# Performance work log

Hardware: AMD Instinct MI355X
Metric: run time of the kernel (lower is better)

## Reference

```python
import jax, jax.numpy as jnp
import numpy as np

ALPHA = 32.0
LN_EPS = 1e-5

def _cdist(a, b):
    # a: [C, M, K], b: [C, N, K] -> [C, M, N] euclidean distances
    d2 = (jnp.sum(a * a, -1)[:, :, None]
          + jnp.sum(b * b, -1)[:, None, :]
          - 2.0 * jnp.einsum('cmk,cnk->cmn', a, b))
    return jnp.sqrt(jnp.maximum(d2, 1e-12))

def setup_inputs() -> dict:
    key = jax.random.key(0)
    k1, k2 = jax.random.split(key)
    B, D, H, W, C = 8, 16, 28, 28, 256
    CN, SS = 128, 28 * 28
    x = jax.random.normal(k1, (B, D, H, W, C), dtype=jnp.float32)
    ln_weight = jnp.ones((C,), dtype=jnp.float32)
    ln_bias = jnp.zeros((C,), dtype=jnp.float32)
    cluster_center = jax.random.uniform(k2, (C, CN, SS), dtype=jnp.float32)
    return {"x": x, "ln_weight": ln_weight, "ln_bias": ln_bias,
            "cluster_center": cluster_center}

def reference(x, ln_weight, ln_bias, cluster_center):
    B, D, H, W, C = x.shape
    CN = cluster_center.shape[1]
    # LayerNorm over last dim (feature_dim)
    mu = jnp.mean(x, -1, keepdims=True)
    var = jnp.mean(jnp.square(x - mu), -1, keepdims=True)
    xn = (x - mu) * jax.lax.rsqrt(var + LN_EPS) * ln_weight + ln_bias
    # B D H W C -> C (B D) (H W)
    x_re = jnp.transpose(xn, (4, 0, 1, 2, 3)).reshape(C, B * D, H * W)
    soft_assign = _cdist(x_re, cluster_center)          # [C, B*D, CN]
    # C (B D) CN -> B D C CN
    x_distance = jnp.transpose(soft_assign.reshape(C, B, D, CN), (1, 2, 0, 3))
    # NegSoftAssign: exp(-alpha*(x - min)) normalized == softmax(-alpha*x)
    x_distance_assign = jax.nn.softmax(-ALPHA * x_distance, axis=-1)
    cluster_dist = _cdist(cluster_center, cluster_center)  # [C, CN, CN]
    return (x_distance, x_distance_assign, cluster_dist)
```

## Files before the change

kernel.cpp:

```cpp
#include <hip/hip_runtime.h>
#include <hip/hip_bf16.h>
#include <math.h>

#define C_DIM 256
#define BD    128
#define HW    784
#define CN    128
#define KPAD  832
#define KTILES 26

typedef short bf16x8 __attribute__((ext_vector_type(8)));
typedef float f32x4 __attribute__((ext_vector_type(4)));

__device__ inline ushort f2b(float f) {
  unsigned u = __float_as_uint(f);
  unsigned r = (u + 0x7FFFu + ((u >> 16) & 1u)) >> 16;
  return (ushort)r;
}

__global__ __launch_bounds__(256) void ln_transpose_kernel(
    const float* __restrict__ x, const float* __restrict__ lnw,
    const float* __restrict__ lnb, ushort* __restrict__ xre,
    float* __restrict__ anorm) {
  __shared__ ushort btile[256 * 64];
  __shared__ float nbuf[4][256];
  const int t = threadIdx.x, bd = blockIdx.y, bx = blockIdx.x;
  const int hw0 = bx * 64;
  const int w = t >> 6, lane = t & 63;
  const int q = lane >> 4, l = lane & 15;
  const bool last = (bx == 12);
  const int ngroups = last ? 1 : 4;
  const int rpw = ngroups * 4;
  if (last) {
    for (int r = 16; r < 64; r += 4)
      *(ushort4*)&btile[t * 64 + r] = make_ushort4(0, 0, 0, 0);
  }
  float4 wv[4], bv[4];
  for (int s = 0; s < 4; ++s) {
    wv[s] = *(const float4*)(lnw + s * 64 + l * 4);
    bv[s] = *(const float4*)(lnb + s * 64 + l * 4);
  }
  float nrm[4][4];
  for (int s = 0; s < 4; ++s)
    for (int j = 0; j < 4; ++j) nrm[s][j] = 0.f;
  const float* xb = x + ((size_t)bd * HW + hw0) * 256 + l * 4;
  const int xr = l & 12;
  for (int g = 0; g < ngroups; ++g) {
    int r = w * rpw + g * 4 + q;
    float4 v[4];
    for (int s = 0; s < 4; ++s)
      v[s] = *(const float4*)(xb + (size_t)r * 256 + s * 64);
    float sum = 0.f, sq = 0.f;
    for (int s = 0; s < 4; ++s) {
      sum += v[s].x + v[s].y + v[s].z + v[s].w;
      sq = fmaf(v[s].x, v[s].x, sq); sq = fmaf(v[s].y, v[s].y, sq);
      sq = fmaf(v[s].z, v[s].z, sq); sq = fmaf(v[s].w, v[s].w, sq);
    }
    for (int off = 1; off <= 8; off <<= 1) {
      sum += __shfl_xor(sum, off, 64);
      sq  += __shfl_xor(sq, off, 64);
    }
    float mu = sum * (1.f / 256.f);
    float var = fmaf(-mu, mu, sq * (1.f / 256.f));
    float sc = rsqrtf(var + 1e-5f);
    int rp = r ^ xr;
    for (int s = 0; s < 4; ++s) {
      float y0 = (v[s].x - mu) * sc * wv[s].x + bv[s].x;
      float y1 = (v[s].y - mu) * sc * wv[s].y + bv[s].y;
      float y2 = (v[s].z - mu) * sc * wv[s].z + bv[s].z;
      float y3 = (v[s].w - mu) * sc * wv[s].w + bv[s].w;
      nrm[s][0] = fmaf(y0, y0, nrm[s][0]);
      nrm[s][1] = fmaf(y1, y1, nrm[s][1]);
      nrm[s][2] = fmaf(y2, y2, nrm[s][2]);
      nrm[s][3] = fmaf(y3, y3, nrm[s][3]);
      int c = s * 64 + l * 4;
      btile[(c + 0) * 64 + rp] = f2b(y0);
      btile[(c + 1) * 64 + rp] = f2b(y1);
      btile[(c + 2) * 64 + rp] = f2b(y2);
      btile[(c + 3) * 64 + rp] = f2b(y3);
    }
  }
  for (int s = 0; s < 4; ++s)
    for (int j = 0; j < 4; ++j) {
      float v = nrm[s][j];
      v += __shfl_xor(v, 16, 64);
      v += __shfl_xor(v, 32, 64);
      nrm[s][j] = v;
    }
  if (q == 0)
    for (int s = 0; s < 4; ++s)
      for (int j = 0; j < 4; ++j) nbuf[w][s * 64 + l * 4 + j] = nrm[s][j];
  __syncthreads();
  float tot = nbuf[0][t] + nbuf[1][t] + nbuf[2][t] + nbuf[3][t];
  atomicAdd(&anorm[t * 128 + bd], tot);
  for (int i = 0; i < 16; ++i) {
    int c = w * 64 + i * 4 + (lane >> 4);
    int xw = (w * 16 + i) & 12;
    int ho = (lane & 15) * 4;
    uint2 val = *(const uint2*)&btile[c * 64 + (ho ^ xw)];
    *(uint2*)(xre + (size_t)c * (BD * KPAD) + (size_t)bd * KPAD + hw0 + ho) = val;
  }
}

__global__ __launch_bounds__(256) void cc_convert_kernel(
    const float* __restrict__ cc, ushort* __restrict__ ccb,
    float* __restrict__ bnorm) {
  int b = blockIdx.x, c = b >> 3;
  int t = threadIdx.x, w = t >> 6, lane = t & 63;
  int q = lane >> 4, l = lane & 15;
  int r = (b & 7) * 16 + w * 4 + q;
  const float4* src = (const float4*)(cc + ((size_t)c * CN + r) * HW);
  ushort* dst = ccb + ((size_t)c * CN + r) * KPAD;
  float nrm = 0.f;
  for (int i = 0; i < 13; ++i) {
    int f = i * 16 + l;
    if (f < 196) {
      float4 v = src[f];
      nrm = fmaf(v.x, v.x, nrm); nrm = fmaf(v.y, v.y, nrm);
      nrm = fmaf(v.z, v.z, nrm); nrm = fmaf(v.w, v.w, nrm);
      ushort4 o; o.x = f2b(v.x); o.y = f2b(v.y); o.z = f2b(v.z); o.w = f2b(v.w);
      *(ushort4*)(dst + f * 4) = o;
    }
  }
  for (int off = 1; off <= 8; off <<= 1) nrm += __shfl_xor(nrm, off, 64);
  if (l == 0) bnorm[c * 128 + r] = nrm;
  if (l < 12) *(ushort4*)(dst + 784 + l * 4) = make_ushort4(0, 0, 0, 0);
}

__global__ __launch_bounds__(512) void gemm_fused_kernel(
    const ushort* __restrict__ xre, const ushort* __restrict__ ccb,
    const float* __restrict__ anorm, const float* __restrict__ bnorm,
    float* __restrict__ out_d, float* __restrict__ out_s,
    float* __restrict__ out_c) {
  __shared__ __align__(16) ushort At[2][4096];
  __shared__ __align__(16) ushort Bt[2][4096];
  const int c = blockIdx.x;
  const int t = threadIdx.x, w = t >> 6, lane = t & 63;
  const int quad = lane >> 4, ln = lane & 15;
  const ushort* Ag = xre + (size_t)c * (128 * KPAD);
  const ushort* Bg = ccb + (size_t)c * (128 * KPAD);

  f32x4 accx[8], accc[8];
  for (int j = 0; j < 8; ++j) {
    accx[j] = f32x4{0.f, 0.f, 0.f, 0.f};
    accc[j] = f32x4{0.f, 0.f, 0.f, 0.f};
  }

  const int srow = t >> 2, scq = (t & 3) ^ (srow & 3);
  const ushort* gA = Ag + (size_t)srow * KPAD + scq * 8;
  const ushort* gB = Bg + (size_t)srow * KPAD + scq * 8;

  const int m = w * 16 + ln;
  const int aoff = (m * 4 + (quad ^ (m & 3))) * 8;
  int boff[8];
#pragma unroll
  for (int j = 0; j < 8; ++j) {
    int n = j * 16 + ln;
    boff[j] = (n * 4 + (quad ^ (n & 3))) * 8;
  }

#define ISSUE(k, p)                                                            \
  do {                                                                         \
    int kb = (k) * 32;                                                         \
    __builtin_amdgcn_global_load_lds(                                          \
        (const __attribute__((address_space(1))) unsigned int*)(gA + kb),      \
        (__attribute__((address_space(3))) unsigned int*)&At[p][t * 8], 16, 0, 0); \
    __builtin_amdgcn_global_load_lds(                                          \
        (const __attribute__((address_space(1))) unsigned int*)(gB + kb),      \
        (__attribute__((address_space(3))) unsigned int*)&Bt[p][t * 8], 16, 0, 0); \
  } while (0)

  ISSUE(0, 0);
  for (int k0 = 0; k0 < KTILES; ++k0) {
    __syncthreads();
    if (k0 < KTILES - 1) ISSUE(k0 + 1, (k0 + 1) & 1);
    const int p = k0 & 1;
    bf16x8 af = *(const bf16x8*)&At[p][aoff];
    bf16x8 ar = *(const bf16x8*)&Bt[p][aoff];
#pragma unroll
    for (int j = 0; j < 8; ++j) {
      bf16x8 bfj = *(const bf16x8*)&Bt[p][boff[j]];
      accx[j] = __builtin_amdgcn_mfma_f32_16x16x32_bf16(af, bfj, accx[j], 0, 0, 0);
      accc[j] = __builtin_amdgcn_mfma_f32_16x16x32_bf16(ar, bfj, accc[j], 0, 0, 0);
    }
  }
#undef ISSUE

  const float* an = anorm + c * 128;
  const float* bn = bnorm + c * 128;
  float cn[8];
  for (int j = 0; j < 8; ++j) cn[j] = bn[j * 16 + ln];
  float rx[4], rc[4];
  for (int r = 0; r < 4; ++r) {
    int mr = w * 16 + quad * 4 + r;
    rx[r] = an[mr];
    rc[r] = bn[mr];
  }
  for (int r = 0; r < 4; ++r) {
    int mr = w * 16 + quad * 4 + r;
    float* ob = out_c + (size_t)c * (128 * 128) + (size_t)mr * 128;
    for (int j = 0; j < 8; ++j) {
      float d2 = rc[r] + cn[j] - 2.f * accc[j][r];
      ob[j * 16 + ln] = sqrtf(fmaxf(d2, 1e-12f));
    }
  }
  for (int r = 0; r < 4; ++r) {
    int mr = w * 16 + quad * 4 + r;
    float dr[8];
    for (int j = 0; j < 8; ++j) {
      float d2 = rx[r] + cn[j] - 2.f * accx[j][r];
      dr[j] = sqrtf(fmaxf(d2, 1e-12f));
    }
    float* ob = out_d + ((size_t)mr * 256 + c) * 128;
    for (int j = 0; j < 8; ++j) ob[j * 16 + ln] = dr[j];
    float mn = dr[0];
    for (int j = 1; j < 8; ++j) mn = fminf(mn, dr[j]);
    for (int off = 1; off <= 8; off <<= 1) mn = fminf(mn, __shfl_xor(mn, off, 64));
    float e[8], s = 0.f;
    for (int j = 0; j < 8; ++j) { e[j] = __expf(-32.f * (dr[j] - mn)); s += e[j]; }
    for (int off = 1; off <= 8; off <<= 1) s += __shfl_xor(s, off, 64);
    float inv = 1.f / s;
    float* os = out_s + ((size_t)mr * 256 + c) * 128;
    for (int j = 0; j < 8; ++j) os[j * 16 + ln] = e[j] * inv;
  }
}

extern "C" void kernel_launch(void* const* d_in, const int* in_sizes, int n_in,
                              void* d_out, int out_size, void* d_ws, size_t ws_size,
                              hipStream_t stream) {
  const float* x   = (const float*)d_in[0];
  const float* lnw = (const float*)d_in[1];
  const float* lnb = (const float*)d_in[2];
  const float* cc  = (const float*)d_in[3];
  float* out   = (float*)d_out;
  float* out_d = out;
  float* out_s = out + 4194304;
  float* out_c = out + 8388608;

  ushort* xre_b = (ushort*)d_ws;
  ushort* cc_b  = xre_b + 27262976;
  float*  anorm = (float*)(cc_b + 27262976);
  float*  bnorm = anorm + 32768;

  hipMemsetAsync(anorm, 0, 32768 * sizeof(float), stream);
  ln_transpose_kernel<<<dim3(13, 128), 256, 0, stream>>>(x, lnw, lnb, xre_b, anorm);
  cc_convert_kernel<<<2048, 256, 0, stream>>>(cc, cc_b, bnorm);
  gemm_fused_kernel<<<256, 512, 0, stream>>>(xre_b, cc_b, anorm, bnorm,
                                             out_d, out_s, out_c);
}
```

Baseline: 295.3 us.

## Merge prep kernels and compute squared norms inside GEMM via MFMA

Combines the LayerNorm-transpose and cluster-center conversion kernels into a single launch with block-index dispatch. It also drops the memset and the global atomics for the norms. Squared norms are now computed inside the GEMM from bf16 operands: one extra MFMA of A with itself gives the diagonal for the row norms, and the existing accc diagonal gives the center norms. The LDS swizzle is changed to reduce bank conflicts, and loads are software-pipelined across row groups. The tradeoff is that the norms now come from bf16-rounded values rather than fp32, which changes accuracy slightly.

```diff
diff --git a/kernel.cpp b/kernel.cpp
--- a/kernel.cpp
+++ b/kernel.cpp
@@ -18,122 +18,129 @@
   return (ushort)r;
 }
 
-__global__ __launch_bounds__(256) void ln_transpose_kernel(
+__global__ __launch_bounds__(256, 4) void prep_kernel(
     const float* __restrict__ x, const float* __restrict__ lnw,
-    const float* __restrict__ lnb, ushort* __restrict__ xre,
-    float* __restrict__ anorm) {
-  __shared__ ushort btile[256 * 64];
-  __shared__ float nbuf[4][256];
-  const int t = threadIdx.x, bd = blockIdx.y, bx = blockIdx.x;
-  const int hw0 = bx * 64;
+    const float* __restrict__ lnb, const float* __restrict__ cc,
+    ushort* __restrict__ xre, ushort* __restrict__ ccb) {
+  __shared__ __align__(16) ushort btile[256 * 64];
+  const int t = threadIdx.x, bid = blockIdx.x;
   const int w = t >> 6, lane = t & 63;
   const int q = lane >> 4, l = lane & 15;
+
+  if (bid < 2048) {
+    const int c = bid >> 3;
+    const int r = (bid & 7) * 16 + w * 4 + q;
+    const float4* src = (const float4*)(cc + ((size_t)c * CN + r) * HW);
+    ushort* dst = ccb + ((size_t)c * CN + r) * KPAD;
+    float4 v[13];
+#pragma unroll
+    for (int i = 0; i < 13; ++i) {
+      if (i < 12 || l < 4) v[i] = src[i * 16 + l];
+    }
+#pragma unroll
+    for (int i = 0; i < 13; ++i) {
+      if (i < 12 || l < 4) {
+        ushort4 o;
+        o.x = f2b(v[i].x); o.y = f2b(v[i].y);
+        o.z = f2b(v[i].z); o.w = f2b(v[i].w);
+        *(ushort4*)(dst + (i * 16 + l) * 4) = o;
+      }
+    }
+    if (l < 12) *(ushort4*)(dst + 784 + l * 4) = make_ushort4(0, 0, 0, 0);
+    return;
+  }
+
+  const int idx = bid - 2048;
+  const int bx = idx % 13;
+  const int bd = idx / 13;
+  const int hw0 = bx * 64;
   const bool last = (bx == 12);
   const int ngroups = last ? 1 : 4;
   const int rpw = ngroups * 4;
+  const int xr2 = (l & 12) | ((l & 3) << 4);
   if (last) {
+    int xf = ((t >> 2) & 12) ^ ((t & 12) << 2);
     for (int r = 16; r < 64; r += 4)
-      *(ushort4*)&btile[t * 64 + r] = make_ushort4(0, 0, 0, 0);
+      *(ushort4*)&btile[t * 64 + (r ^ xf)] = make_ushort4(0, 0, 0, 0);
   }
   float4 wv[4], bv[4];
+#pragma unroll
   for (int s = 0; s < 4; ++s) {
     wv[s] = *(const float4*)(lnw + s * 64 + l * 4);
     bv[s] = *(const float4*)(lnb + s * 64 + l * 4);
   }
-  float nrm[4][4];
-  for (int s = 0; s < 4; ++s)
-    for (int j = 0; j < 4; ++j) nrm[s][j] = 0.f;
   const float* xb = x + ((size_t)bd * HW + hw0) * 256 + l * 4;
-  const int xr = l & 12;
-  for (int g = 0; g < ngroups; ++g) {
-    int r = w * rpw + g * 4 + q;
-    float4 v[4];
-    for (int s = 0; s < 4; ++s)
-      v[s] = *(const float4*)(xb + (size_t)r * 256 + s * 64);
-    float sum = 0.f, sq = 0.f;
-    for (int s = 0; s < 4; ++s) {
-      sum += v[s].x + v[s].y + v[s].z + v[s].w;
-      sq = fmaf(v[s].x, v[s].x, sq); sq = fmaf(v[s].y, v[s].y, sq);
-      sq = fmaf(v[s].z, v[s].z, sq); sq = fmaf(v[s].w, v[s].w, sq);
-    }
-    for (int off = 1; off <= 8; off <<= 1) {
-      sum += __shfl_xor(sum, off, 64);
-      sq  += __shfl_xor(sq, off, 64);
-    }
-    float mu = sum * (1.f / 256.f);
-    float var = fmaf(-mu, mu, sq * (1.f / 256.f));
-    float sc = rsqrtf(var + 1e-5f);
-    int rp = r ^ xr;
-    for (int s = 0; s < 4; ++s) {
-      float y0 = (v[s].x - mu) * sc * wv[s].x + bv[s].x;
-      float y1 = (v[s].y - mu) * sc * wv[s].y + bv[s].y;
-      float y2 = (v[s].z - mu) * sc * wv[s].z + bv[s].z;
-      float y3 = (v[s].w - mu) * sc * wv[s].w + bv[s].w;
-      nrm[s][0] = fmaf(y0, y0, nrm[s][0]);
-      nrm[s][1] = fmaf(y1, y1, nrm[s][1]);
-      nrm[s][2] = fmaf(y2, y2, nrm[s][2]);
-      nrm[s][3] = fmaf(y3, y3, nrm[s][3]);
-      int c = s * 64 + l * 4;
-      btile[(c + 0) * 64 + rp] = f2b(y0);
-      btile[(c + 1) * 64 + rp] = f2b(y1);
-      btile[(c + 2) * 64 + rp] = f2b(y2);
-      btile[(c + 3) * 64 + rp] = f2b(y3);
-    }
-  }
-  for (int s = 0; s < 4; ++s)
-    for (int j = 0; j < 4; ++j) {
-      float v = nrm[s][j];
-      v += __shfl_xor(v, 16, 64);
-      v += __shfl_xor(v, 32, 64);
-      nrm[s][j] = v;
-    }
-  if (q == 0)
-    for (int s = 0; s < 4; ++s)
-      for (int j = 0; j < 4; ++j) nbuf[w][s * 64 + l * 4 + j] = nrm[s][j];
+
+#define LOADG(V, g)                                                            \
+  do {                                                                         \
+    int r_ = w * rpw + (g) * 4 + q;                                            \
+    _Pragma("unroll") for (int s = 0; s < 4; ++s)                              \
+        V[s] = *(const float4*)(xb + (size_t)r_ * 256 + s * 64);               \
+  } while (0)
+
+#define PROC(V, g)                                                             \
+  do {                                                                         \
+    int r_ = w * rpw + (g) * 4 + q;                                            \
+    float sum = 0.f, sq = 0.f;                                                 \
+    _Pragma("unroll") for (int s = 0; s < 4; ++s) {                            \
+      sum += V[s].x + V[s].y + V[s].z + V[s].w;                                \
+      sq = fmaf(V[s].x, V[s].x, sq); sq = fmaf(V[s].y, V[s].y, sq);            \
+      sq = fmaf(V[s].z, V[s].z, sq); sq = fmaf(V[s].w, V[s].w, sq);            \
+    }                                                                          \
+    for (int off = 1; off <= 8; off <<= 1) {                                   \
+      sum += __shfl_xor(sum, off, 64);                                         \
+      sq  += __shfl_xor(sq, off, 64);                                          \
+    }                                                                          \
+    float mu = sum * (1.f / 256.f);                                            \
+    float var = fmaf(-mu, mu, sq * (1.f / 256.f));                             \
+    float sc = rsqrtf(var + 1e-5f);                                            \
+    int rp_ = r_ ^ xr2;                                                        \
+    _Pragma("unroll") for (int s = 0; s < 4; ++s) {                            \
+      float y0 = (V[s].x - mu) * sc * wv[s].x + bv[s].x;                       \
+      float y1 = (V[s].y - mu) * sc * wv[s].y + bv[s].y;                       \
+      float y2 = (V[s].z - mu) * sc * wv[s].z + bv[s].z;                       \
+      float y3 = (V[s].w - mu) * sc * wv[s].w + bv[s].w;                       \
+      int c_ = s * 64 + l * 4;                                                 \
+      btile[(c_ + 0) * 64 + rp_] = f2b(y0);                                    \
+      btile[(c_ + 1) * 64 + rp_] = f2b(y1);                                    \
+      btile[(c_ + 2) * 64 + rp_] = f2b(y2);                                    \
+      btile[(c_ + 3) * 64 + rp_] = f2b(y3);                                    \
+    }                                                                          \
+  } while (0)
+
+  float4 va[4], vb[4];
+  LOADG(va, 0);
+  if (ngroups > 1) {
+    LOADG(vb, 1);
+    PROC(va, 0);
+    LOADG(va, 2);
+    PROC(vb, 1);
+    LOADG(vb, 3);
+    PROC(va, 2);
+    PROC(vb, 3);
+  } else {
+    PROC(va, 0);
+  }
+#undef LOADG
+#undef PROC
   __syncthreads();
-  float tot = nbuf[0][t] + nbuf[1][t] + nbuf[2][t] + nbuf[3][t];
-  atomicAdd(&anorm[t * 128 + bd], tot);
+#pragma unroll
   for (int i = 0; i < 16; ++i) {
     int c = w * 64 + i * 4 + (lane >> 4);
-    int xw = (w * 16 + i) & 12;
+    int xw = ((c >> 2) & 12) ^ ((c & 12) << 2);
     int ho = (lane & 15) * 4;
     uint2 val = *(const uint2*)&btile[c * 64 + (ho ^ xw)];
     *(uint2*)(xre + (size_t)c * (BD * KPAD) + (size_t)bd * KPAD + hw0 + ho) = val;
   }
 }
 
-__global__ __launch_bounds__(256) void cc_convert_kernel(
-    const float* __restrict__ cc, ushort* __restrict__ ccb,
-    float* __restrict__ bnorm) {
-  int b = blockIdx.x, c = b >> 3;
-  int t = threadIdx.x, w = t >> 6, lane = t & 63;
-  int q = lane >> 4, l = lane & 15;
-  int r = (b & 7) * 16 + w * 4 + q;
-  const float4* src = (const float4*)(cc + ((size_t)c * CN + r) * HW);
-  ushort* dst = ccb + ((size_t)c * CN + r) * KPAD;
-  float nrm = 0.f;
-  for (int i = 0; i < 13; ++i) {
-    int f = i * 16 + l;
-    if (f < 196) {
-      float4 v = src[f];
-      nrm = fmaf(v.x, v.x, nrm); nrm = fmaf(v.y, v.y, nrm);
-      nrm = fmaf(v.z, v.z, nrm); nrm = fmaf(v.w, v.w, nrm);
-      ushort4 o; o.x = f2b(v.x); o.y = f2b(v.y); o.z = f2b(v.z); o.w = f2b(v.w);
-      *(ushort4*)(dst + f * 4) = o;
-    }
-  }
-  for (int off = 1; off <= 8; off <<= 1) nrm += __shfl_xor(nrm, off, 64);
-  if (l == 0) bnorm[c * 128 + r] = nrm;
-  if (l < 12) *(ushort4*)(dst + 784 + l * 4) = make_ushort4(0, 0, 0, 0);
-}
-
 __global__ __launch_bounds__(512) void gemm_fused_kernel(
     const ushort* __restrict__ xre, const ushort* __restrict__ ccb,
-    const float* __restrict__ anorm, const float* __restrict__ bnorm,
     float* __restrict__ out_d, float* __restrict__ out_s,
     float* __restrict__ out_c) {
   __shared__ __align__(16) ushort At[2][4096];
   __shared__ __align__(16) ushort Bt[2][4096];
+  __shared__ float an_l[128], bn_l[128];
   const int c = blockIdx.x;
   const int t = threadIdx.x, w = t >> 6, lane = t & 63;
   const int quad = lane >> 4, ln = lane & 15;
@@ -141,6 +148,7 @@
   const ushort* Bg = ccb + (size_t)c * (128 * KPAD);
 
   f32x4 accx[8], accc[8];
+  f32x4 accd = f32x4{0.f, 0.f, 0.f, 0.f};
   for (int j = 0; j < 8; ++j) {
     accx[j] = f32x4{0.f, 0.f, 0.f, 0.f};
     accc[j] = f32x4{0.f, 0.f, 0.f, 0.f};
@@ -177,6 +185,7 @@
     const int p = k0 & 1;
     bf16x8 af = *(const bf16x8*)&At[p][aoff];
     bf16x8 ar = *(const bf16x8*)&Bt[p][aoff];
+    accd = __builtin_amdgcn_mfma_f32_16x16x32_bf16(af, af, accd, 0, 0, 0);
 #pragma unroll
     for (int j = 0; j < 8; ++j) {
       bf16x8 bfj = *(const bf16x8*)&Bt[p][boff[j]];
@@ -186,15 +195,19 @@
   }
 #undef ISSUE
 
-  const float* an = anorm + c * 128;
-  const float* bn = bnorm + c * 128;
+  if ((ln >> 2) == quad) {
+    an_l[w * 16 + ln] = accd[ln & 3];
+    bn_l[w * 16 + ln] = accc[w][ln & 3];
+  }
+  __syncthreads();
+
   float cn[8];
-  for (int j = 0; j < 8; ++j) cn[j] = bn[j * 16 + ln];
+  for (int j = 0; j < 8; ++j) cn[j] = bn_l[j * 16 + ln];
   float rx[4], rc[4];
   for (int r = 0; r < 4; ++r) {
-    int mr = w * 16 + quad * 4 + r;
-    rx[r] = an[mr];
-    rc[r] = bn[mr];
+    int p16 = quad * 4 + r;
+    rx[r] = an_l[w * 16 + p16];
+    rc[r] = bn_l[w * 16 + p16];
   }
   for (int r = 0; r < 4; ++r) {
     int mr = w * 16 + quad * 4 + r;
@@ -239,12 +252,7 @@
 
   ushort* xre_b = (ushort*)d_ws;
   ushort* cc_b  = xre_b + 27262976;
-  float*  anorm = (float*)(cc_b + 27262976);
-  float*  bnorm = anorm + 32768;
-
-  hipMemsetAsync(anorm, 0, 32768 * sizeof(float), stream);
-  ln_transpose_kernel<<<dim3(13, 128), 256, 0, stream>>>(x, lnw, lnb, xre_b, anorm);
-  cc_convert_kernel<<<2048, 256, 0, stream>>>(cc, cc_b, bnorm);
-  gemm_fused_kernel<<<256, 512, 0, stream>>>(xre_b, cc_b, anorm, bnorm,
-                                             out_d, out_s, out_c);
-}
+
+  prep_kernel<<<3712, 256, 0, stream>>>(x, lnw, lnb, cc, xre_b, cc_b);
+  gemm_fused_kernel<<<256, 512, 0, stream>>>(xre_b, cc_b, out_d, out_s, out_c);
+}
```

Result: faster. 288.4 us (-2.3%).
